# Optimization experiments

Hardware: AMD Instinct MI355X
Metric: run time of the kernel (lower is better)

The kernel has to match this reference:

```python
import jax, jax.numpy as jnp
from jax import lax
import numpy as np

B, T, D_IN, H, OUT = 64, 512, 512, 1024, 128


def setup_inputs() -> dict:
    key = jax.random.key(0)
    ks = jax.random.split(key, 12)
    s = 0.02
    return {
        "x": jax.random.normal(ks[0], (B, T, D_IN), dtype=jnp.float32),
        "W_ih0": jax.random.normal(ks[1], (H, D_IN), dtype=jnp.float32) * s,
        "W_hh0": jax.random.normal(ks[2], (H, H), dtype=jnp.float32) * s,
        "b_ih0": jax.random.normal(ks[3], (H,), dtype=jnp.float32) * s,
        "b_hh0": jax.random.normal(ks[4], (H,), dtype=jnp.float32) * s,
        "W_ih1": jax.random.normal(ks[5], (H, H), dtype=jnp.float32) * s,
        "W_hh1": jax.random.normal(ks[6], (H, H), dtype=jnp.float32) * s,
        "b_ih1": jax.random.normal(ks[7], (H,), dtype=jnp.float32) * s,
        "b_hh1": jax.random.normal(ks[8], (H,), dtype=jnp.float32) * s,
        "W_fc": jax.random.normal(ks[9], (OUT, H), dtype=jnp.float32) * s,
        "b_fc": jax.random.normal(ks[10], (OUT,), dtype=jnp.float32) * s,
    }


def _rnn_layer(seq, W_ih, W_hh, b_ih, b_hh):
    # seq: [B, T, D] -> outputs [B, T, H]; h_t = tanh(x_t W_ih^T + b_ih + h_{t-1} W_hh^T + b_hh)
    pre = jnp.einsum("btd,hd->bth", seq, W_ih) + b_ih + b_hh  # one big input GEMM
    h0 = jnp.zeros((seq.shape[0], W_hh.shape[0]), dtype=seq.dtype)

    def step(h, p_t):
        h_new = jnp.tanh(p_t + h @ W_hh.T)
        return h_new, h_new

    _, hs = lax.scan(step, h0, jnp.swapaxes(pre, 0, 1))  # [T, B, H]
    return jnp.swapaxes(hs, 0, 1)  # [B, T, H]


def reference(x, W_ih0, W_hh0, b_ih0, b_hh0, W_ih1, W_hh1, b_ih1, b_hh1, W_fc, b_fc):
    h1 = _rnn_layer(x, W_ih0, W_hh0, b_ih0, b_hh0)
    h2 = _rnn_layer(h1, W_ih1, W_hh1, b_ih1, b_hh1)
    last = h2[:, -1, :]  # [B, H]
    return last @ W_fc.T + b_fc  # [B, OUT]
```

## Files before the change

### kernel.cpp

```cpp
#include <hip/hip_runtime.h>
#include <stdint.h>
#include <stddef.h>

#define Bn   64
#define Tn   512
#define DINn 512
#define Hn   1024
#define OUTn 128

typedef __attribute__((ext_vector_type(4))) float f32x4;
typedef __attribute__((ext_vector_type(8))) short short8;
typedef __attribute__((ext_vector_type(4))) unsigned int u32x4;

__device__ __forceinline__ unsigned short f2bf(float f){
  unsigned int x = __builtin_bit_cast(unsigned int, f);
  x += 0x7fffu + ((x >> 16) & 1u);
  return (unsigned short)(x >> 16);
}
__device__ __forceinline__ float bf2f(unsigned short u){
  return __builtin_bit_cast(float, (unsigned int)u << 16);
}
__device__ __forceinline__ float tanh_fast(float v){
  float e = __expf(2.0f * v);
  return 1.0f - 2.0f / (e + 1.0f);
}

template<bool FAST>
__device__ __forceinline__ void st16(unsigned short* p, u32x4 v){
  if constexpr (FAST)
    asm volatile("global_store_dwordx4 %0, %1, off sc0" :: "v"(p), "v"(v) : "memory");
  else
    asm volatile("global_store_dwordx4 %0, %1, off sc0 sc1" :: "v"(p), "v"(v) : "memory");
}
__device__ __forceinline__ unsigned atom_poll(unsigned int* p){
  unsigned old, zero = 0;
  asm volatile("global_atomic_add %0, %1, %2, off sc0\n\t"
               "s_waitcnt vmcnt(0)"
               : "=&v"(old) : "v"(p), "v"(zero) : "memory");
  return old;
}
__device__ __forceinline__ void atom_poll2(unsigned int* p1, unsigned int* p2,
                                           unsigned &v1, unsigned &v2){
  unsigned zero = 0;
  asm volatile("global_atomic_add %0, %2, %4, off sc0\n\t"
               "global_atomic_add %1, %3, %4, off sc0\n\t"
               "s_waitcnt vmcnt(0)"
               : "=&v"(v1), "=&v"(v2)
               : "v"(p1), "v"(p2), "v"(zero) : "memory");
}
__device__ __forceinline__ void atom_inc(unsigned int* p){
  unsigned one = 1;
  asm volatile("global_atomic_add %0, %1, off" :: "v"(p), "v"(one) : "memory");
}
__device__ __forceinline__ unsigned ld1_sc0(const unsigned int* p){
  unsigned v;
  asm volatile("global_load_dword %0, %1, off sc0\n\t"
               "s_waitcnt vmcnt(0)" : "=&v"(v) : "v"(p) : "memory");
  return v;
}
__device__ __forceinline__ unsigned ld1_nt(const unsigned int* p){
  unsigned v;
  asm volatile("global_load_dword %0, %1, off nt\n\t"
               "s_waitcnt vmcnt(0)" : "=&v"(v) : "v"(p) : "memory");
  return v;
}
__device__ __forceinline__ unsigned umin4(u32x4 a){
  unsigned m0 = a[0] < a[1] ? a[0] : a[1];
  unsigned m1 = a[2] < a[3] ? a[2] : a[3];
  return m0 < m1 ? m0 : m1;
}
__device__ __forceinline__ unsigned ld_line8_nt(const unsigned int* p){
  u32x4 a, b;
  asm volatile("global_load_dwordx4 %0, %2, off nt\n\t"
               "global_load_dwordx4 %1, %3, off nt\n\t"
               "s_waitcnt vmcnt(0)"
               : "=&v"(a), "=&v"(b) : "v"(p), "v"(p + 4) : "memory");
  unsigned ma = umin4(a), mb = umin4(b);
  return ma < mb ? ma : mb;
}
__device__ __forceinline__ unsigned ld_line8_slow(const unsigned int* p){
  u32x4 a, b;
  asm volatile("global_load_dwordx4 %0, %2, off sc0 sc1\n\t"
               "global_load_dwordx4 %1, %3, off sc0 sc1\n\t"
               "s_waitcnt vmcnt(0)"
               : "=&v"(a), "=&v"(b) : "v"(p), "v"(p + 4) : "memory");
  unsigned ma = umin4(a), mb = umin4(b);
  return ma < mb ? ma : mb;
}
__device__ __forceinline__ void wait8_nt(const unsigned int* p, unsigned want){
  if (!want) return;
  for (int i = 0; i < (1 << 16); ++i){
    if (ld_line8_nt(p) >= want) return;
    if (i > 16) __builtin_amdgcn_s_sleep(1);
  }
}
__device__ __forceinline__ void wait8_nt2(const unsigned int* p1, unsigned w1,
                                          const unsigned int* p2, unsigned w2){
  if (!w1){ wait8_nt(p2, w2); return; }
  for (int i = 0; i < (1 << 16); ++i){
    u32x4 a, b, c, d;
    asm volatile("global_load_dwordx4 %0, %4, off nt\n\t"
                 "global_load_dwordx4 %1, %5, off nt\n\t"
                 "global_load_dwordx4 %2, %6, off nt\n\t"
                 "global_load_dwordx4 %3, %7, off nt\n\t"
                 "s_waitcnt vmcnt(0)"
                 : "=&v"(a), "=&v"(b), "=&v"(c), "=&v"(d)
                 : "v"(p1), "v"(p1 + 4), "v"(p2), "v"(p2 + 4) : "memory");
    unsigned m1 = umin4(a) < umin4(b) ? umin4(a) : umin4(b);
    unsigned m2 = umin4(c) < umin4(d) ? umin4(c) : umin4(d);
    if (m1 >= w1 && m2 >= w2) return;
    if (i > 16) __builtin_amdgcn_s_sleep(1);
  }
}
template<bool FAST>
__device__ __forceinline__ void wait_one(unsigned int* fc, unsigned int* fl, unsigned wfast, unsigned wslow){
  if constexpr (FAST){
    if (!wfast) return;
    for (int i = 0; i < (1 << 16); ++i){
      if (atom_poll(fc) >= wfast) return;
      if (i > 8) __builtin_amdgcn_s_sleep(1);
    }
  } else {
    if (!wslow) return;
    for (int i = 0; i < (1 << 16); ++i){
      if (ld_line8_slow(fl) >= wslow) return;
      if (i > 16) __builtin_amdgcn_s_sleep(1);
    }
  }
}
template<bool FAST>
__device__ __forceinline__ void wait_dual(unsigned int* fc1, unsigned int* fl1, unsigned wf1, unsigned ws1,
                                          unsigned int* fc2, unsigned int* fl2, unsigned wf2, unsigned ws2){
  if constexpr (FAST){
    if (!wf2){ wait_one<true>(fc1, fl1, wf1, ws1); return; }
    for (int i = 0; i < (1 << 16); ++i){
      unsigned v1, v2;
      atom_poll2(fc1, fc2, v1, v2);
      if (v1 >= wf1 && v2 >= wf2) return;
      if (i > 8) __builtin_amdgcn_s_sleep(1);
    }
  } else {
    if (!ws2){ wait_one<false>(fc1, fl1, wf1, ws1); return; }
    for (int i = 0; i < (1 << 16); ++i){
      if (ld_line8_slow(fl1) >= ws1 && ld_line8_slow(fl2) >= ws2) return;
      if (i > 16) __builtin_amdgcn_s_sleep(1);
    }
  }
}

__device__ __forceinline__ void stage_pw(const unsigned short* src, unsigned short* dst, int lane){
  const unsigned short* p0 = src + lane*8;
  const unsigned short* p1 = p0 + 512;
  u32x4 v0, v1;
  asm volatile("global_load_dwordx4 %0, %2, off sc0\n\t"
               "global_load_dwordx4 %1, %3, off sc0\n\t"
               "s_waitcnt vmcnt(0)"
               : "=&v"(v0), "=&v"(v1) : "v"(p0), "v"(p1) : "memory");
  *(u32x4*)(dst + lane*8) = v0;
  *(u32x4*)(dst + lane*8 + 512) = v1;
}
__device__ __forceinline__ void stage_pw_pv(const unsigned short* src, unsigned short* dst, int lane,
                                            const unsigned short* p4, float* pv){
  const unsigned short* p0 = src + lane*8;
  const unsigned short* p1 = p0 + 512;
  u32x4 v0, v1; unsigned u0,u1,u2,u3;
  asm volatile(
    "global_load_dwordx4 %0, %6, off sc0\n\t"
    "global_load_dwordx4 %1, %7, off sc0\n\t"
    "global_load_ushort %2, %8, off sc0\n\t"
    "global_load_ushort %3, %9, off sc0\n\t"
    "global_load_ushort %4, %10, off sc0\n\t"
    "global_load_ushort %5, %11, off sc0\n\t"
    "s_waitcnt vmcnt(0)"
    : "=&v"(v0),"=&v"(v1),"=&v"(u0),"=&v"(u1),"=&v"(u2),"=&v"(u3)
    : "v"(p0),"v"(p1),"v"(p4),"v"(p4+8),"v"(p4+16),"v"(p4+24) : "memory");
  *(u32x4*)(dst + lane*8) = v0;
  *(u32x4*)(dst + lane*8 + 512) = v1;
  pv[0]=bf2f((unsigned short)u0); pv[1]=bf2f((unsigned short)u1);
  pv[2]=bf2f((unsigned short)u2); pv[3]=bf2f((unsigned short)u3);
}

template<bool FAST>
__device__ __forceinline__ void stage_lin(const unsigned short* base, unsigned short* hl, int tid){
  const unsigned short* p0 = base + (size_t)tid * 8;
  const unsigned short* p1 = p0 + 4096;
  u32x4 v0, v1;
  if constexpr (FAST)
    asm volatile("global_load_dwordx4 %0, %2, off sc0\n\t"
                 "global_load_dwordx4 %1, %3, off sc0\n\t"
                 "s_waitcnt vmcnt(0)"
                 : "=&v"(v0), "=&v"(v1) : "v"(p0), "v"(p1) : "memory");
  else
    asm volatile("global_load_dwordx4 %0, %2, off sc0 sc1\n\t"
                 "global_load_dwordx4 %1, %3, off sc0 sc1\n\t"
                 "s_waitcnt vmcnt(0)"
                 : "=&v"(v0), "=&v"(v1) : "v"(p0), "v"(p1) : "memory");
  *(u32x4*)((char*)hl + tid * 16) = v0;
  *(u32x4*)((char*)hl + tid * 16 + 8192) = v1;
}
template<bool FAST>
__device__ __forceinline__ void ld4_chunk(const unsigned short* p, float* pv){
  unsigned u0,u1,u2,u3;
  if constexpr (FAST)
    asm volatile("global_load_ushort %0, %4, off sc0\n\t"
                 "global_load_ushort %1, %5, off sc0\n\t"
                 "global_load_ushort %2, %6, off sc0\n\t"
                 "global_load_ushort %3, %7, off sc0\n\t"
                 "s_waitcnt vmcnt(0)"
                 : "=&v"(u0), "=&v"(u1), "=&v"(u2), "=&v"(u3)
                 : "v"(p), "v"(p + 8), "v"(p + 16), "v"(p + 24) : "memory");
  else
    asm volatile("global_load_ushort %0, %4, off sc0 sc1\n\t"
                 "global_load_ushort %1, %5, off sc0 sc1\n\t"
                 "global_load_ushort %2, %6, off sc0 sc1\n\t"
                 "global_load_ushort %3, %7, off sc0 sc1\n\t"
                 "s_waitcnt vmcnt(0)"
                 : "=&v"(u0), "=&v"(u1), "=&v"(u2), "=&v"(u3)
                 : "v"(p), "v"(p + 8), "v"(p + 16), "v"(p + 24) : "memory");
  pv[0] = bf2f((unsigned short)u0); pv[1] = bf2f((unsigned short)u1);
  pv[2] = bf2f((unsigned short)u2); pv[3] = bf2f((unsigned short)u3);
}

__device__ __forceinline__ f32x4 mfma_tile(const char* lbase, const short8* wf, int lrow, int kh){
  f32x4 a0 = {0.f,0.f,0.f,0.f}, a1 = a0, a2 = a0, a3 = a0;
  int rb = kh * 128 + lrow * 16;
#pragma unroll
  for (int kk = 0; kk < 8; ++kk)
    a0 = __builtin_amdgcn_mfma_f32_16x16x32_bf16(*(const short8*)(lbase + kk*512 + rb), wf[kk], a0, 0,0,0);
#pragma unroll
  for (int kk = 8; kk < 16; ++kk)
    a1 = __builtin_amdgcn_mfma_f32_16x16x32_bf16(*(const short8*)(lbase + kk*512 + rb), wf[kk], a1, 0,0,0);
#pragma unroll
  for (int kk = 16; kk < 24; ++kk)
    a2 = __builtin_amdgcn_mfma_f32_16x16x32_bf16(*(const short8*)(lbase + kk*512 + rb), wf[kk], a2, 0,0,0);
#pragma unroll
  for (int kk = 24; kk < 32; ++kk)
    a3 = __builtin_amdgcn_mfma_f32_16x16x32_bf16(*(const short8*)(lbase + kk*512 + rb), wf[kk], a3, 0,0,0);
  return (a0 + a1) + (a2 + a3);
}

__global__ void cvt_bf16x8(const float* __restrict__ in, unsigned short* __restrict__ out,
                           long long n8){
  long long i = (long long)blockIdx.x * blockDim.x + threadIdx.x;
  long long stride = (long long)gridDim.x * blockDim.x;
  for (; i < n8; i += stride){
    const float* p = in + i*8;
    float4 a = *(const float4*)p;
    float4 b = *(const float4*)(p+4);
    short8 v;
    v[0]=(short)f2bf(a.x); v[1]=(short)f2bf(a.y); v[2]=(short)f2bf(a.z); v[3]=(short)f2bf(a.w);
    v[4]=(short)f2bf(b.x); v[5]=(short)f2bf(b.y); v[6]=(short)f2bf(b.z); v[7]=(short)f2bf(b.w);
    *(short8*)(out + i*8) = v;
  }
}

__global__ void bias_combine(const float* __restrict__ a, const float* __restrict__ b, float* __restrict__ o,
                             const float* __restrict__ c, const float* __restrict__ d, float* __restrict__ p){
  int i = blockIdx.x * blockDim.x + threadIdx.x;
  if (i < Hn){ o[i] = a[i] + b[i]; p[i] = c[i] + d[i]; }
}

__launch_bounds__(256, 2)
__global__ void gemm_pre0(const float* __restrict__ Av, const unsigned short* __restrict__ Bm,
                          const float* __restrict__ bias, unsigned short* __restrict__ C,
                          int N, int K)
{
  __shared__ unsigned short lA[128*64];
  __shared__ unsigned short lB[128*64];
  int bn = blockIdx.x, bm = blockIdx.y;
  int m0 = bm*128, n0 = bn*128;
  int tid = threadIdx.x, lane = tid & 63, w = tid >> 6;
  int wm = (w >> 1)*64, wn = (w & 1)*64;
  int cl = lane & 15, kh = lane >> 4;

  f32x4 acc[4][4];
  f32x4 z = {0.f,0.f,0.f,0.f};
#pragma unroll
  for (int i=0;i<4;i++)
#pragma unroll
    for (int j=0;j<4;j++) acc[i][j]=z;

  for (int k0 = 0; k0 < K; k0 += 64){
    __syncthreads();
#pragma unroll
    for (int r = 0; r < 4; ++r){
      int c = r*256 + tid;
      int row = c >> 3, cof = (c & 7)*8;
      const float* ap = Av + (size_t)(m0+row)*K + k0 + cof;
      float4 a = *(const float4*)ap;
      float4 b = *(const float4*)(ap+4);
      short8 v;
      v[0]=(short)f2bf(a.x); v[1]=(short)f2bf(a.y); v[2]=(short)f2bf(a.z); v[3]=(short)f2bf(a.w);
      v[4]=(short)f2bf(b.x); v[5]=(short)f2bf(b.y); v[6]=(short)f2bf(b.z); v[7]=(short)f2bf(b.w);
      *(short8*)&lA[row*64 + cof] = v;
      const unsigned short* bp = Bm + (size_t)(n0+row)*K + k0 + cof;
      *(short8*)&lB[row*64 + cof] = *(const short8*)bp;
    }
    __syncthreads();
#pragma unroll
    for (int kk = 0; kk < 2; ++kk){
      int kb = kk*32 + kh*8;
      short8 af[4], bfr[4];
#pragma unroll
      for (int i=0;i<4;i++) af[i]  = *(const short8*)&lA[(wm + i*16 + cl)*64 + kb];
#pragma unroll
      for (int j=0;j<4;j++) bfr[j] = *(const short8*)&lB[(wn + j*16 + cl)*64 + kb];
#pragma unroll
      for (int i=0;i<4;i++)
#pragma unroll
        for (int j=0;j<4;j++)
          acc[i][j] = __builtin_amdgcn_mfma_f32_16x16x32_bf16(af[i], bfr[j], acc[i][j], 0,0,0);
    }
  }
#pragma unroll
  for (int j=0;j<4;j++){
    int n = n0 + wn + j*16 + cl;
    float bs = bias[n];
#pragma unroll
    for (int i=0;i<4;i++){
      int mr = m0 + wm + i*16 + kh*4;
#pragma unroll
      for (int e=0;e<4;e++){
        int m = mr + e;
        int b = m >> 9, t = m & (Tn-1);
        C[((size_t)t*Bn + b)*N + n] = f2bf(acc[i][j][e] + bs);
      }
    }
  }
}

template<int MODE>
__device__ __forceinline__ void rnn_body(
    int role, int g, int slot, int tid, int w, int lane, int cl, int kh, int lrow,
    const unsigned short* pre0, unsigned short* bufP, unsigned short* h1buf,
    const float* bias1,
    unsigned int* FCA0, unsigned int* FCA1, unsigned int* FCB, unsigned int* FCC,
    unsigned int* FLA, unsigned int* FLB, unsigned int* FLC,
    unsigned int* FNA, unsigned int* FNB, unsigned int* FNC,
    const short8* wf, unsigned short* hl, unsigned short* outl)
{
  constexpr bool FAST = (MODE < 2);
  int n0 = slot*128 + w*16;
  int olocal = w*128 + ((cl>>3)*8 + kh*4)*8 + (cl&7);
  int khc = kh & 1;
  unsigned int* myFL = ((role == 0) ? FLA : (role == 1) ? FLB : FLC) + slot;
  unsigned int* myFN = ((role == 0) ? FNA : (role == 1) ? FNB : FNC) + slot*8 + w;

  for (int t = 0; t < Tn; ++t){
    unsigned short* hlb = (MODE == 0) ? hl + (t & 1)*8192 : hl;
    const char* lbase = (const char*)hlb;

    float pv[4] = {0.f,0.f,0.f,0.f};
    if (role == 0 && kh < 2){
      const unsigned short* pp = pre0 + ((size_t)t*Bn + g*8 + kh*4)*Hn + n0 + cl;
#pragma unroll
      for (int j=0;j<4;j++) pv[j] = bf2f(pp[(size_t)j*Hn]);
    }
    bool staged = true;
    if constexpr (MODE == 0){
      if (role == 0){
        if (t > 0){
          wait8_nt(FNA + w*8, (unsigned)t);
          stage_pw(h1buf + ((size_t)(t+1)*8 + g)*8192 + w*1024, hlb + w*1024, lane);
        } else staged = false;
      } else if (role == 1){
        wait8_nt(FNA + w*8, (unsigned)(t+1));
        stage_pw(h1buf + ((size_t)(t+2)*8 + g)*8192 + w*1024, hlb + w*1024, lane);
      } else {
        const unsigned short* pA = h1buf + ((size_t)t*8 + g)*8192 + slot*1024
                                   + ((w*16+cl)>>3)*64 + khc*32 + (cl&7);
        if (t > 0){
          wait8_nt2(FNC + w*8, (unsigned)t, FNB + slot*8, (unsigned)(t+1));
          stage_pw_pv(bufP + ((size_t)(t-1)*Bn + g*8)*Hn + w*1024, hlb + w*1024, lane, pA, pv);
        } else {
          staged = false;
          wait8_nt(FNB + slot*8, 1u);
          ld4_chunk<true>(pA, pv);
        }
      }
    } else {
      if (tid == 0){
        if (role == 0)      wait_one <FAST>(FCA0, FLA, 8u*(unsigned)t, (unsigned)t);
        else if (role == 1) wait_one <FAST>(FCA1, FLA, 8u*(unsigned)(t+1), (unsigned)(t+1));
        else                wait_dual<FAST>(FCB, FLB, 8u*(unsigned)(t+1), (unsigned)(t+1),
                                            FCC, FLC, 8u*(unsigned)t, (unsigned)t);
      }
      __syncthreads();
      if (role == 0){
        if (t > 0) stage_lin<FAST>(h1buf + ((size_t)(t+1)*8 + g)*8192, hlb, tid);
        else staged = false;
      } else if (role == 1){
        stage_lin<FAST>(h1buf + ((size_t)(t+2)*8 + g)*8192, hlb, tid);
      } else {
        if (kh < 2)
          ld4_chunk<FAST>(h1buf + ((size_t)t*8 + g)*8192 + slot*1024 + ((w*16+cl)>>3)*64 + kh*32 + (cl&7), pv);
        if (t > 0) stage_lin<FAST>(bufP + ((size_t)(t-1)*Bn + g*8)*Hn, hlb, tid);
        else staged = false;
      }
    }
    __syncthreads();
    f32x4 acc = {0.f,0.f,0.f,0.f};
    if (staged) acc = mfma_tile(lbase, wf, lrow, kh);
    if (kh < 2){
      float bs = (role == 1) ? bias1[n0 + cl] : 0.f;
#pragma unroll
      for (int j=0;j<4;j++){
        float v = acc[j] + pv[j] + bs;
        if (role != 1) v = tanh_fast(v);
        outl[olocal + j*8] = f2bf(v);
      }
    }
    unsigned short* tile;
    if (role == 0)      tile = h1buf + ((size_t)(t+2)*8 + g)*8192;
    else if (role == 1) tile = h1buf + ((size_t)t*8 + g)*8192;
    else                tile = bufP + ((size_t)t*Bn + g*8)*Hn;
    if (lane < 16){
      u32x4 v = *(const u32x4*)(outl + w*128 + lane*8);
      st16<FAST>(tile + slot*1024 + (w*16 + lane)*8, v);
    }
    if constexpr (MODE == 0){
      asm volatile("s_waitcnt vmcnt(0)" ::: "memory");
      if (lane == 0)
        asm volatile("global_store_dword %0, %1, off sc0" :: "v"(myFN), "v"((unsigned)(t+1)) : "memory");
    } else {
      asm volatile("s_waitcnt vmcnt(0)" ::: "memory");
      __syncthreads();
      if (tid == 0){
        if constexpr (MODE == 1){
          if (role == 0){ atom_inc(FCA0); atom_inc(FCA1); }
          else if (role == 1) atom_inc(FCB);
          else atom_inc(FCC);
        } else {
          asm volatile("global_store_dword %0, %1, off sc0 sc1" :: "v"(myFL), "v"((unsigned)(t+1)) : "memory");
        }
      }
    }
  }
}

__launch_bounds__(512, 2)
__global__ void rnn_fused(const unsigned short* __restrict__ pre0_ro,
                          unsigned short* __restrict__ bufP,
                          unsigned short* __restrict__ h1buf,
                          const float* __restrict__ Whh0,
                          const float* __restrict__ Wih1,
                          const float* __restrict__ Whh1,
                          const float* __restrict__ bias1,
                          unsigned int* ctrs)
{
  __shared__ __align__(16) unsigned short hl[16384];
  __shared__ __align__(16) unsigned short outl[1024];
  __shared__ int s_mode;
  int bx = blockIdx.x;
  int g = bx & 7;
  int sub = bx >> 3;
  int role = sub >> 3, slot = sub & 7;
  int tid = threadIdx.x, lane = tid & 63, w = tid >> 6;
  int n0 = slot*128 + w*16;
  int cl = lane & 15, kh = lane >> 4, lrow = cl & 7;
  unsigned int* FLA = ctrs + (0*8 + g)*32;
  unsigned int* FLB = ctrs + (1*8 + g)*32;
  unsigned int* FLC = ctrs + (2*8 + g)*32;
  unsigned int* arrive1 = ctrs + 768;
  unsigned int* badAT   = ctrs + 772;
  unsigned int* arrive2 = ctrs + 776;
  unsigned int* badNT   = ctrs + 780;
  unsigned int* arrive3 = ctrs + 784;
  unsigned int* FCA0 = ctrs + 1536 + (0*8 + g)*32;
  unsigned int* FCB  = ctrs + 1536 + (1*8 + g)*32;
  unsigned int* FCC  = ctrs + 1536 + (2*8 + g)*32;
  unsigned int* FCA1 = ctrs + 1536 + (3*8 + g)*32;
  unsigned int* FNA = ctrs + 2560 + (0*8 + g)*64;
  unsigned int* FNB = ctrs + 2560 + (1*8 + g)*64;
  unsigned int* FNC = ctrs + 2560 + (2*8 + g)*64;

  if (tid == 0){
    int xcc;
    asm volatile("s_getreg_b32 %0, hwreg(HW_REG_XCC_ID)" : "=s"(xcc));
    unsigned int* atw = ctrs + 1024 + g*32;  unsigned int* atarmed = atw + 16;
    unsigned int* ntw = ctrs + 1280 + g*32;  unsigned int* ntarmed = ntw + 16;
    if (xcc != g){
      __hip_atomic_fetch_or(badNT, 1u, __ATOMIC_RELAXED, __HIP_MEMORY_SCOPE_AGENT);
      __hip_atomic_fetch_or(badAT, 1u, __ATOMIC_RELAXED, __HIP_MEMORY_SCOPE_AGENT);
    }
    unsigned pr = ld1_nt(ntw) + ld1_nt(ntarmed);
    asm volatile("" :: "v"(pr));
    __hip_atomic_fetch_add(arrive1, 1u, __ATOMIC_ACQ_REL, __HIP_MEMORY_SCOPE_AGENT);
    int t1 = 0;
    for (int i = 0; i < (1 << 20); ++i){
      if (__hip_atomic_load(arrive1, __ATOMIC_ACQUIRE, __HIP_MEMORY_SCOPE_AGENT) >= 192u){ t1 = 1; break; }
      __builtin_amdgcn_s_sleep(2);
    }
    if (!t1){
      __hip_atomic_fetch_or(badNT, 1u, __ATOMIC_RELAXED, __HIP_MEMORY_SCOPE_AGENT);
      __hip_atomic_fetch_or(badAT, 1u, __ATOMIC_RELAXED, __HIP_MEMORY_SCOPE_AGENT);
    }
    unsigned magicN = 0xBEEF0000u | (unsigned)g;
    if (sub == 0){
      asm volatile("global_store_dword %0, %1, off sc0\n\t"
                   "s_waitcnt vmcnt(0)\n\t"
                   "global_store_dword %2, %3, off sc0"
                   :: "v"(ntw), "v"(magicN), "v"(ntarmed), "v"(1u) : "memory");
    }
    int okN = 0;
    for (int i = 0; i < (1 << 14); ++i){
      if (ld1_nt(ntarmed) == 1u){ okN = (ld1_nt(ntw) == magicN); break; }
      if (i > 8) __builtin_amdgcn_s_sleep(1);
    }
    if (!okN) __hip_atomic_fetch_or(badNT, 1u, __ATOMIC_RELAXED, __HIP_MEMORY_SCOPE_AGENT);
    __hip_atomic_fetch_add(arrive2, 1u, __ATOMIC_ACQ_REL, __HIP_MEMORY_SCOPE_AGENT);
    int t2 = 0;
    for (int i = 0; i < (1 << 20); ++i){
      if (__hip_atomic_load(arrive2, __ATOMIC_ACQUIRE, __HIP_MEMORY_SCOPE_AGENT) >= 192u){ t2 = 1; break; }
      __builtin_amdgcn_s_sleep(2);
    }
    if (!t2){
      __hip_atomic_fetch_or(badNT, 1u, __ATOMIC_RELAXED, __HIP_MEMORY_SCOPE_AGENT);
      __hip_atomic_fetch_or(badAT, 1u, __ATOMIC_RELAXED, __HIP_MEMORY_SCOPE_AGENT);
    }
    unsigned magicA = 0xCAFE0000u | (unsigned)g;
    if (sub == 0){
      asm volatile("global_store_dword %0, %1, off sc0\n\t"
                   "s_waitcnt vmcnt(0)" :: "v"(atw), "v"(magicA) : "memory");
      atom_inc(atarmed);
    }
    int okA = 0;
    for (int i = 0; i < (1 << 15); ++i){
      if (atom_poll(atarmed) >= 1u){ okA = (ld1_sc0(atw) == magicA); break; }
      if (i > 16) __builtin_amdgcn_s_sleep(1);
    }
    if (!okA) __hip_atomic_fetch_or(badAT, 1u, __ATOMIC_RELAXED, __HIP_MEMORY_SCOPE_AGENT);
    __hip_atomic_fetch_add(arrive3, 1u, __ATOMIC_ACQ_REL, __HIP_MEMORY_SCOPE_AGENT);
    int t3 = 0;
    for (int i = 0; i < (1 << 20); ++i){
      if (__hip_atomic_load(arrive3, __ATOMIC_ACQUIRE, __HIP_MEMORY_SCOPE_AGENT) >= 192u){ t3 = 1; break; }
      __builtin_amdgcn_s_sleep(2);
    }
    unsigned bN = __hip_atomic_load(badNT, __ATOMIC_ACQUIRE, __HIP_MEMORY_SCOPE_AGENT);
    unsigned bA = __hip_atomic_load(badAT, __ATOMIC_ACQUIRE, __HIP_MEMORY_SCOPE_AGENT);
    s_mode = (!t3) ? 2 : (bN == 0u ? 0 : (bA == 0u ? 1 : 2));
  }
  __syncthreads();
  const int mode = s_mode;

  const float* Wmat = (role == 0) ? Whh0 : (role == 1) ? Wih1 : Whh1;
  short8 wf[32];
  {
    const float* wr = Wmat + (size_t)(n0 + cl)*Hn + kh*8;
#pragma unroll
    for (int kk = 0; kk < 32; ++kk){
      float4 a = *(const float4*)(wr + kk*32);
      float4 b = *(const float4*)(wr + kk*32 + 4);
      short8 v;
      v[0]=(short)f2bf(a.x); v[1]=(short)f2bf(a.y); v[2]=(short)f2bf(a.z); v[3]=(short)f2bf(a.w);
      v[4]=(short)f2bf(b.x); v[5]=(short)f2bf(b.y); v[6]=(short)f2bf(b.z); v[7]=(short)f2bf(b.w);
      wf[kk] = v;
    }
  }

  if (mode == 0)
    rnn_body<0>(role, g, slot, tid, w, lane, cl, kh, lrow, pre0_ro, bufP, h1buf,
                bias1, FCA0, FCA1, FCB, FCC, FLA, FLB, FLC, FNA, FNB, FNC, wf, hl, outl);
  else if (mode == 1)
    rnn_body<1>(role, g, slot, tid, w, lane, cl, kh, lrow, pre0_ro, bufP, h1buf,
                bias1, FCA0, FCA1, FCB, FCC, FLA, FLB, FLC, FNA, FNB, FNC, wf, hl, outl);
  else
    rnn_body<2>(role, g, slot, tid, w, lane, cl, kh, lrow, pre0_ro, bufP, h1buf,
                bias1, FCA0, FCA1, FCB, FCC, FLA, FLB, FLC, FNA, FNB, FNC, wf, hl, outl);
}

__global__ void fc_k(const unsigned short* __restrict__ bufP,
                     const float* __restrict__ Wfc, const float* __restrict__ bfc,
                     float* __restrict__ out)
{
  int gw = (blockIdx.x * blockDim.x + threadIdx.x) >> 6;
  int lane = threadIdx.x & 63;
  int b = gw >> 7, o = gw & 127;
  const unsigned short* tile = bufP + ((size_t)(Tn-1)*Bn + (b & ~7))*Hn;
  int r = b & 7;
  const float* wr = Wfc + (size_t)o*Hn;
  float s = 0.f;
  for (int k = lane; k < Hn; k += 64)
    s += bf2f(tile[((k>>3)*8 + r)*8 + (k&7)]) * wr[k];
#pragma unroll
  for (int off = 32; off > 0; off >>= 1) s += __shfl_down(s, off, 64);
  if (lane == 0) out[b*OUTn + o] = s + bfc[o];
}

extern "C" void kernel_launch(void* const* d_in, const int* in_sizes, int n_in,
                              void* d_out, int out_size, void* d_ws, size_t ws_size,
                              hipStream_t stream)
{
  const float* x    = (const float*)d_in[0];
  const float* Wih0 = (const float*)d_in[1];
  const float* Whh0 = (const float*)d_in[2];
  const float* bih0 = (const float*)d_in[3];
  const float* bhh0 = (const float*)d_in[4];
  const float* Wih1 = (const float*)d_in[5];
  const float* Whh1 = (const float*)d_in[6];
  const float* bih1 = (const float*)d_in[7];
  const float* bhh1 = (const float*)d_in[8];
  const float* Wfc  = (const float*)d_in[9];
  const float* bfc  = (const float*)d_in[10];
  float* out = (float*)d_out;

  unsigned short* bufP  = (unsigned short*)d_ws;
  unsigned short* h1buf = bufP  + (size_t)Bn*Tn*Hn;
  unsigned short* wih0b = h1buf + (size_t)(Tn+2)*8*8192;
  float* bias0 = (float*)(wih0b + (size_t)Hn*DINn);
  float* bias1 = bias0 + Hn;
  unsigned int* ctrs = (unsigned int*)(bias1 + Hn);

  hipMemsetAsync(ctrs, 0, 4096*sizeof(unsigned int), stream);

  cvt_bf16x8<<<256, 256, 0, stream>>>(Wih0, wih0b, (long long)Hn*DINn/8);
  bias_combine<<<4, 256, 0, stream>>>(bih0, bhh0, bias0, bih1, bhh1, bias1);

  dim3 g1(Hn/128, (Bn*Tn)/128);
  gemm_pre0<<<g1, 256, 0, stream>>>(x, wih0b, bias0, bufP, Hn, DINn);

  rnn_fused<<<192, 512, 0, stream>>>(bufP, bufP, h1buf, Whh0, Wih1, Whh1, bias1, ctrs);

  fc_k<<<2048, 256, 0, stream>>>(bufP, Wfc, bfc, out);
}
```

Measured before the change: 1.127 ms.

## Halve waves per RNN block, each wave computing two 16-column tiles

The persistent RNN kernel now launches 256 threads per block instead of 512. Each of the 4 waves holds two sets of bf16 weight fragments and computes 32 output columns through interleaved MFMA chains. Staging loads widen to four dwordx4 per lane, and the per-wave flag layout and polling shrink to match. This cuts the number of waves that sync and poll per step, but doubles register pressure for the weights (64 short8 per lane) and lengthens each wave's serial MFMA work.

```diff
diff --git a/kernel.cpp b/kernel.cpp
--- a/kernel.cpp
+++ b/kernel.cpp
@@ -87,6 +87,13 @@
   unsigned ma = umin4(a), mb = umin4(b);
   return ma < mb ? ma : mb;
 }
+__device__ __forceinline__ void waitw_nt(const unsigned int* p, unsigned want){
+  if (!want) return;
+  for (int i = 0; i < (1 << 16); ++i){
+    if (ld1_nt(p) >= want) return;
+    if (i > 16) __builtin_amdgcn_s_sleep(1);
+  }
+}
 __device__ __forceinline__ void wait8_nt(const unsigned int* p, unsigned want){
   if (!want) return;
   for (int i = 0; i < (1 << 16); ++i){
@@ -94,21 +101,18 @@
     if (i > 16) __builtin_amdgcn_s_sleep(1);
   }
 }
-__device__ __forceinline__ void wait8_nt2(const unsigned int* p1, unsigned w1,
-                                          const unsigned int* p2, unsigned w2){
-  if (!w1){ wait8_nt(p2, w2); return; }
+__device__ __forceinline__ void waitC_nt(const unsigned int* pline, unsigned wline,
+                                         const unsigned int* pw, unsigned ww){
   for (int i = 0; i < (1 << 16); ++i){
-    u32x4 a, b, c, d;
-    asm volatile("global_load_dwordx4 %0, %4, off nt\n\t"
-                 "global_load_dwordx4 %1, %5, off nt\n\t"
-                 "global_load_dwordx4 %2, %6, off nt\n\t"
-                 "global_load_dwordx4 %3, %7, off nt\n\t"
+    u32x4 a, b; unsigned v;
+    asm volatile("global_load_dwordx4 %0, %3, off nt\n\t"
+                 "global_load_dwordx4 %1, %4, off nt\n\t"
+                 "global_load_dword %2, %5, off nt\n\t"
                  "s_waitcnt vmcnt(0)"
-                 : "=&v"(a), "=&v"(b), "=&v"(c), "=&v"(d)
-                 : "v"(p1), "v"(p1 + 4), "v"(p2), "v"(p2 + 4) : "memory");
-    unsigned m1 = umin4(a) < umin4(b) ? umin4(a) : umin4(b);
-    unsigned m2 = umin4(c) < umin4(d) ? umin4(c) : umin4(d);
-    if (m1 >= w1 && m2 >= w2) return;
+                 : "=&v"(a), "=&v"(b), "=&v"(v)
+                 : "v"(pline), "v"(pline + 4), "v"(pw) : "memory");
+    unsigned m = umin4(a) < umin4(b) ? umin4(a) : umin4(b);
+    if (m >= wline && v >= ww) return;
     if (i > 16) __builtin_amdgcn_s_sleep(1);
   }
 }
@@ -148,55 +152,79 @@
   }
 }
 
-__device__ __forceinline__ void stage_pw(const unsigned short* src, unsigned short* dst, int lane){
+__device__ __forceinline__ void stage_pw4k(const unsigned short* src, unsigned short* dst, int lane){
   const unsigned short* p0 = src + lane*8;
-  const unsigned short* p1 = p0 + 512;
-  u32x4 v0, v1;
-  asm volatile("global_load_dwordx4 %0, %2, off sc0\n\t"
-               "global_load_dwordx4 %1, %3, off sc0\n\t"
+  u32x4 v0, v1, v2, v3;
+  asm volatile("global_load_dwordx4 %0, %4, off sc0\n\t"
+               "global_load_dwordx4 %1, %5, off sc0\n\t"
+               "global_load_dwordx4 %2, %6, off sc0\n\t"
+               "global_load_dwordx4 %3, %7, off sc0\n\t"
                "s_waitcnt vmcnt(0)"
-               : "=&v"(v0), "=&v"(v1) : "v"(p0), "v"(p1) : "memory");
+               : "=&v"(v0), "=&v"(v1), "=&v"(v2), "=&v"(v3)
+               : "v"(p0), "v"(p0 + 512), "v"(p0 + 1024), "v"(p0 + 1536) : "memory");
   *(u32x4*)(dst + lane*8) = v0;
   *(u32x4*)(dst + lane*8 + 512) = v1;
-}
-__device__ __forceinline__ void stage_pw_pv(const unsigned short* src, unsigned short* dst, int lane,
-                                            const unsigned short* p4, float* pv){
+  *(u32x4*)(dst + lane*8 + 1024) = v2;
+  *(u32x4*)(dst + lane*8 + 1536) = v3;
+}
+__device__ __forceinline__ void stage_pw4k_pv(const unsigned short* src, unsigned short* dst, int lane,
+                                              const unsigned short* pA, const unsigned short* pB,
+                                              float* pvA, float* pvB){
   const unsigned short* p0 = src + lane*8;
-  const unsigned short* p1 = p0 + 512;
-  u32x4 v0, v1; unsigned u0,u1,u2,u3;
+  u32x4 v0, v1, v2, v3;
+  unsigned a0,a1,a2,a3,b0,b1,b2,b3;
   asm volatile(
-    "global_load_dwordx4 %0, %6, off sc0\n\t"
-    "global_load_dwordx4 %1, %7, off sc0\n\t"
-    "global_load_ushort %2, %8, off sc0\n\t"
-    "global_load_ushort %3, %9, off sc0\n\t"
-    "global_load_ushort %4, %10, off sc0\n\t"
-    "global_load_ushort %5, %11, off sc0\n\t"
+    "global_load_dwordx4 %0, %12, off sc0\n\t"
+    "global_load_dwordx4 %1, %13, off sc0\n\t"
+    "global_load_dwordx4 %2, %14, off sc0\n\t"
+    "global_load_dwordx4 %3, %15, off sc0\n\t"
+    "global_load_ushort %4, %16, off sc0\n\t"
+    "global_load_ushort %5, %17, off sc0\n\t"
+    "global_load_ushort %6, %18, off sc0\n\t"
+    "global_load_ushort %7, %19, off sc0\n\t"
+    "global_load_ushort %8, %20, off sc0\n\t"
+    "global_load_ushort %9, %21, off sc0\n\t"
+    "global_load_ushort %10, %22, off sc0\n\t"
+    "global_load_ushort %11, %23, off sc0\n\t"
     "s_waitcnt vmcnt(0)"
-    : "=&v"(v0),"=&v"(v1),"=&v"(u0),"=&v"(u1),"=&v"(u2),"=&v"(u3)
-    : "v"(p0),"v"(p1),"v"(p4),"v"(p4+8),"v"(p4+16),"v"(p4+24) : "memory");
+    : "=&v"(v0),"=&v"(v1),"=&v"(v2),"=&v"(v3),
+      "=&v"(a0),"=&v"(a1),"=&v"(a2),"=&v"(a3),"=&v"(b0),"=&v"(b1),"=&v"(b2),"=&v"(b3)
+    : "v"(p0), "v"(p0+512), "v"(p0+1024), "v"(p0+1536),
+      "v"(pA),"v"(pA+8),"v"(pA+16),"v"(pA+24),
+      "v"(pB),"v"(pB+8),"v"(pB+16),"v"(pB+24) : "memory");
   *(u32x4*)(dst + lane*8) = v0;
   *(u32x4*)(dst + lane*8 + 512) = v1;
-  pv[0]=bf2f((unsigned short)u0); pv[1]=bf2f((unsigned short)u1);
-  pv[2]=bf2f((unsigned short)u2); pv[3]=bf2f((unsigned short)u3);
-}
-
+  *(u32x4*)(dst + lane*8 + 1024) = v2;
+  *(u32x4*)(dst + lane*8 + 1536) = v3;
+  pvA[0]=bf2f((unsigned short)a0); pvA[1]=bf2f((unsigned short)a1);
+  pvA[2]=bf2f((unsigned short)a2); pvA[3]=bf2f((unsigned short)a3);
+  pvB[0]=bf2f((unsigned short)b0); pvB[1]=bf2f((unsigned short)b1);
+  pvB[2]=bf2f((unsigned short)b2); pvB[3]=bf2f((unsigned short)b3);
+}
 template<bool FAST>
-__device__ __forceinline__ void stage_lin(const unsigned short* base, unsigned short* hl, int tid){
+__device__ __forceinline__ void stage_lin4(const unsigned short* base, unsigned short* hl, int tid){
   const unsigned short* p0 = base + (size_t)tid * 8;
-  const unsigned short* p1 = p0 + 4096;
-  u32x4 v0, v1;
+  u32x4 v0, v1, v2, v3;
   if constexpr (FAST)
-    asm volatile("global_load_dwordx4 %0, %2, off sc0\n\t"
-                 "global_load_dwordx4 %1, %3, off sc0\n\t"
+    asm volatile("global_load_dwordx4 %0, %4, off sc0\n\t"
+                 "global_load_dwordx4 %1, %5, off sc0\n\t"
+                 "global_load_dwordx4 %2, %6, off sc0\n\t"
+                 "global_load_dwordx4 %3, %7, off sc0\n\t"
                  "s_waitcnt vmcnt(0)"
-                 : "=&v"(v0), "=&v"(v1) : "v"(p0), "v"(p1) : "memory");
+                 : "=&v"(v0), "=&v"(v1), "=&v"(v2), "=&v"(v3)
+                 : "v"(p0), "v"(p0+2048), "v"(p0+4096), "v"(p0+6144) : "memory");
   else
-    asm volatile("global_load_dwordx4 %0, %2, off sc0 sc1\n\t"
-                 "global_load_dwordx4 %1, %3, off sc0 sc1\n\t"
+    asm volatile("global_load_dwordx4 %0, %4, off sc0 sc1\n\t"
+                 "global_load_dwordx4 %1, %5, off sc0 sc1\n\t"
+                 "global_load_dwordx4 %2, %6, off sc0 sc1\n\t"
+                 "global_load_dwordx4 %3, %7, off sc0 sc1\n\t"
                  "s_waitcnt vmcnt(0)"
-                 : "=&v"(v0), "=&v"(v1) : "v"(p0), "v"(p1) : "memory");
-  *(u32x4*)((char*)hl + tid * 16) = v0;
-  *(u32x4*)((char*)hl + tid * 16 + 8192) = v1;
+                 : "=&v"(v0), "=&v"(v1), "=&v"(v2), "=&v"(v3)
+                 : "v"(p0), "v"(p0+2048), "v"(p0+4096), "v"(p0+6144) : "memory");
+  *(u32x4*)(hl + tid*8) = v0;
+  *(u32x4*)(hl + tid*8 + 2048) = v1;
+  *(u32x4*)(hl + tid*8 + 4096) = v2;
+  *(u32x4*)(hl + tid*8 + 6144) = v3;
 }
 template<bool FAST>
 __device__ __forceinline__ void ld4_chunk(const unsigned short* p, float* pv){
@@ -221,22 +249,21 @@
   pv[2] = bf2f((unsigned short)u2); pv[3] = bf2f((unsigned short)u3);
 }
 
-__device__ __forceinline__ f32x4 mfma_tile(const char* lbase, const short8* wf, int lrow, int kh){
-  f32x4 a0 = {0.f,0.f,0.f,0.f}, a1 = a0, a2 = a0, a3 = a0;
+__device__ __forceinline__ void mfma_tile2(const char* lbase, const short8* wfA, const short8* wfB,
+                                           int lrow, int kh, f32x4& outA, f32x4& outB){
+  f32x4 z = {0.f,0.f,0.f,0.f};
+  f32x4 a0 = z, a1 = z, b0 = z, b1 = z;
   int rb = kh * 128 + lrow * 16;
 #pragma unroll
-  for (int kk = 0; kk < 8; ++kk)
-    a0 = __builtin_amdgcn_mfma_f32_16x16x32_bf16(*(const short8*)(lbase + kk*512 + rb), wf[kk], a0, 0,0,0);
-#pragma unroll
-  for (int kk = 8; kk < 16; ++kk)
-    a1 = __builtin_amdgcn_mfma_f32_16x16x32_bf16(*(const short8*)(lbase + kk*512 + rb), wf[kk], a1, 0,0,0);
-#pragma unroll
-  for (int kk = 16; kk < 24; ++kk)
-    a2 = __builtin_amdgcn_mfma_f32_16x16x32_bf16(*(const short8*)(lbase + kk*512 + rb), wf[kk], a2, 0,0,0);
-#pragma unroll
-  for (int kk = 24; kk < 32; ++kk)
-    a3 = __builtin_amdgcn_mfma_f32_16x16x32_bf16(*(const short8*)(lbase + kk*512 + rb), wf[kk], a3, 0,0,0);
-  return (a0 + a1) + (a2 + a3);
+  for (int kk = 0; kk < 32; kk += 2){
+    short8 x = *(const short8*)(lbase + kk*512 + rb);
+    short8 y = *(const short8*)(lbase + (kk+1)*512 + rb);
+    a0 = __builtin_amdgcn_mfma_f32_16x16x32_bf16(x, wfA[kk],   a0, 0,0,0);
+    b0 = __builtin_amdgcn_mfma_f32_16x16x32_bf16(x, wfB[kk],   b0, 0,0,0);
+    a1 = __builtin_amdgcn_mfma_f32_16x16x32_bf16(y, wfA[kk+1], a1, 0,0,0);
+    b1 = __builtin_amdgcn_mfma_f32_16x16x32_bf16(y, wfB[kk+1], b1, 0,0,0);
+  }
+  outA = a0 + a1; outB = b0 + b1;
 }
 
 __global__ void cvt_bf16x8(const float* __restrict__ in, unsigned short* __restrict__ out,
@@ -337,45 +364,50 @@
     unsigned int* FCA0, unsigned int* FCA1, unsigned int* FCB, unsigned int* FCC,
     unsigned int* FLA, unsigned int* FLB, unsigned int* FLC,
     unsigned int* FNA, unsigned int* FNB, unsigned int* FNC,
-    const short8* wf, unsigned short* hl, unsigned short* outl)
+    const short8* wfA, const short8* wfB, unsigned short* hl, unsigned short* outl)
 {
   constexpr bool FAST = (MODE < 2);
-  int n0 = slot*128 + w*16;
-  int olocal = w*128 + ((cl>>3)*8 + kh*4)*8 + (cl&7);
+  int c0 = slot*128 + 32*w;
+  int olocal = w*256 + ((cl>>3)*8 + kh*4)*8 + (cl&7);
   int khc = kh & 1;
   unsigned int* myFL = ((role == 0) ? FLA : (role == 1) ? FLB : FLC) + slot;
-  unsigned int* myFN = ((role == 0) ? FNA : (role == 1) ? FNB : FNC) + slot*8 + w;
+  unsigned int* myFN = ((role == 0) ? FNA : (role == 1) ? FNB : FNC) + slot*4 + w;
+
+  float bsA = 0.f, bsB = 0.f;
+  if (role == 1){ bsA = bias1[c0 + cl]; bsB = bias1[c0 + 16 + cl]; }
 
   for (int t = 0; t < Tn; ++t){
     unsigned short* hlb = (MODE == 0) ? hl + (t & 1)*8192 : hl;
     const char* lbase = (const char*)hlb;
 
-    float pv[4] = {0.f,0.f,0.f,0.f};
+    float pvA[4] = {0.f,0.f,0.f,0.f}, pvB[4] = {0.f,0.f,0.f,0.f};
     if (role == 0 && kh < 2){
-      const unsigned short* pp = pre0 + ((size_t)t*Bn + g*8 + kh*4)*Hn + n0 + cl;
-#pragma unroll
-      for (int j=0;j<4;j++) pv[j] = bf2f(pp[(size_t)j*Hn]);
+      const unsigned short* pp = pre0 + ((size_t)t*Bn + g*8 + kh*4)*Hn + c0 + cl;
+#pragma unroll
+      for (int j=0;j<4;j++){ pvA[j] = bf2f(pp[(size_t)j*Hn]); pvB[j] = bf2f(pp[(size_t)j*Hn + 16]); }
     }
     bool staged = true;
     if constexpr (MODE == 0){
       if (role == 0){
         if (t > 0){
           wait8_nt(FNA + w*8, (unsigned)t);
-          stage_pw(h1buf + ((size_t)(t+1)*8 + g)*8192 + w*1024, hlb + w*1024, lane);
+          stage_pw4k(h1buf + ((size_t)(t+1)*8 + g)*8192 + 2*w*1024, hlb + 2*w*1024, lane);
         } else staged = false;
       } else if (role == 1){
         wait8_nt(FNA + w*8, (unsigned)(t+1));
-        stage_pw(h1buf + ((size_t)(t+2)*8 + g)*8192 + w*1024, hlb + w*1024, lane);
+        stage_pw4k(h1buf + ((size_t)(t+2)*8 + g)*8192 + 2*w*1024, hlb + 2*w*1024, lane);
       } else {
-        const unsigned short* pA = h1buf + ((size_t)t*8 + g)*8192 + slot*1024
-                                   + ((w*16+cl)>>3)*64 + khc*32 + (cl&7);
+        const unsigned short* pb = h1buf + ((size_t)t*8 + g)*8192 + slot*1024;
+        const unsigned short* pA = pb + ((c0 - slot*128 + cl) >> 3)*64 + khc*32 + (cl & 7);
+        const unsigned short* pB = pA + 128;
         if (t > 0){
-          wait8_nt2(FNC + w*8, (unsigned)t, FNB + slot*8, (unsigned)(t+1));
-          stage_pw_pv(bufP + ((size_t)(t-1)*Bn + g*8)*Hn + w*1024, hlb + w*1024, lane, pA, pv);
+          waitC_nt(FNC + w*8, (unsigned)t, FNB + slot*4 + w, (unsigned)(t+1));
+          stage_pw4k_pv(bufP + ((size_t)(t-1)*Bn + g*8)*Hn + 2*w*1024, hlb + 2*w*1024, lane,
+                        pA, pB, pvA, pvB);
         } else {
           staged = false;
-          wait8_nt(FNB + slot*8, 1u);
-          ld4_chunk<true>(pA, pv);
+          waitw_nt(FNB + slot*4 + w, 1u);
+          ld4_chunk<true>(pA, pvA); ld4_chunk<true>(pB, pvB);
         }
       }
     } else {
@@ -387,36 +419,39 @@
       }
       __syncthreads();
       if (role == 0){
-        if (t > 0) stage_lin<FAST>(h1buf + ((size_t)(t+1)*8 + g)*8192, hlb, tid);
+        if (t > 0) stage_lin4<FAST>(h1buf + ((size_t)(t+1)*8 + g)*8192, hlb, tid);
         else staged = false;
       } else if (role == 1){
-        stage_lin<FAST>(h1buf + ((size_t)(t+2)*8 + g)*8192, hlb, tid);
+        stage_lin4<FAST>(h1buf + ((size_t)(t+2)*8 + g)*8192, hlb, tid);
       } else {
-        if (kh < 2)
-          ld4_chunk<FAST>(h1buf + ((size_t)t*8 + g)*8192 + slot*1024 + ((w*16+cl)>>3)*64 + kh*32 + (cl&7), pv);
-        if (t > 0) stage_lin<FAST>(bufP + ((size_t)(t-1)*Bn + g*8)*Hn, hlb, tid);
+        const unsigned short* pb = h1buf + ((size_t)t*8 + g)*8192 + slot*1024;
+        const unsigned short* pA = pb + ((32*w + cl) >> 3)*64 + kh*32 + (cl & 7);
+        if (kh < 2){ ld4_chunk<FAST>(pA, pvA); ld4_chunk<FAST>(pA + 128, pvB); }
+        if (t > 0) stage_lin4<FAST>(bufP + ((size_t)(t-1)*Bn + g*8)*Hn, hlb, tid);
         else staged = false;
       }
     }
     __syncthreads();
-    f32x4 acc = {0.f,0.f,0.f,0.f};
-    if (staged) acc = mfma_tile(lbase, wf, lrow, kh);
+    f32x4 accA = {0.f,0.f,0.f,0.f}, accB = accA;
+    if (staged) mfma_tile2(lbase, wfA, wfB, lrow, kh, accA, accB);
     if (kh < 2){
-      float bs = (role == 1) ? bias1[n0 + cl] : 0.f;
 #pragma unroll
       for (int j=0;j<4;j++){
-        float v = acc[j] + pv[j] + bs;
-        if (role != 1) v = tanh_fast(v);
-        outl[olocal + j*8] = f2bf(v);
+        float vA = accA[j] + pvA[j] + bsA;
+        float vB = accB[j] + pvB[j] + bsB;
+        if (role != 1){ vA = tanh_fast(vA); vB = tanh_fast(vB); }
+        outl[olocal + j*8]       = f2bf(vA);
+        outl[olocal + 128 + j*8] = f2bf(vB);
       }
     }
     unsigned short* tile;
     if (role == 0)      tile = h1buf + ((size_t)(t+2)*8 + g)*8192;
     else if (role == 1) tile = h1buf + ((size_t)t*8 + g)*8192;
     else                tile = bufP + ((size_t)t*Bn + g*8)*Hn;
+    tile += slot*1024;
     if (lane < 16){
-      u32x4 v = *(const u32x4*)(outl + w*128 + lane*8);
-      st16<FAST>(tile + slot*1024 + (w*16 + lane)*8, v);
+      st16<FAST>(tile + (32*w + lane)*8,      *(const u32x4*)(outl + w*256 + lane*8));
+      st16<FAST>(tile + (32*w + 16 + lane)*8, *(const u32x4*)(outl + w*256 + 128 + lane*8));
     }
     if constexpr (MODE == 0){
       asm volatile("s_waitcnt vmcnt(0)" ::: "memory");
@@ -438,7 +473,7 @@
   }
 }
 
-__launch_bounds__(512, 2)
+__launch_bounds__(256, 1)
 __global__ void rnn_fused(const unsigned short* __restrict__ pre0_ro,
                           unsigned short* __restrict__ bufP,
                           unsigned short* __restrict__ h1buf,
@@ -456,7 +491,6 @@
   int sub = bx >> 3;
   int role = sub >> 3, slot = sub & 7;
   int tid = threadIdx.x, lane = tid & 63, w = tid >> 6;
-  int n0 = slot*128 + w*16;
   int cl = lane & 15, kh = lane >> 4, lrow = cl & 7;
   unsigned int* FLA = ctrs + (0*8 + g)*32;
   unsigned int* FLB = ctrs + (1*8 + g)*32;
@@ -470,9 +504,9 @@
   unsigned int* FCB  = ctrs + 1536 + (1*8 + g)*32;
   unsigned int* FCC  = ctrs + 1536 + (2*8 + g)*32;
   unsigned int* FCA1 = ctrs + 1536 + (3*8 + g)*32;
-  unsigned int* FNA = ctrs + 2560 + (0*8 + g)*64;
-  unsigned int* FNB = ctrs + 2560 + (1*8 + g)*64;
-  unsigned int* FNC = ctrs + 2560 + (2*8 + g)*64;
+  unsigned int* FNA = ctrs + 2560 + (0*8 + g)*32;
+  unsigned int* FNB = ctrs + 2560 + (1*8 + g)*32;
+  unsigned int* FNC = ctrs + 2560 + (2*8 + g)*32;
 
   if (tid == 0){
     int xcc;
@@ -544,29 +578,41 @@
   const int mode = s_mode;
 
   const float* Wmat = (role == 0) ? Whh0 : (role == 1) ? Wih1 : Whh1;
-  short8 wf[32];
+  int c0 = slot*128 + 32*w;
+  short8 wfA[32], wfB[32];
   {
-    const float* wr = Wmat + (size_t)(n0 + cl)*Hn + kh*8;
+    const float* wrA = Wmat + (size_t)(c0 + cl)*Hn + kh*8;
+    const float* wrB = wrA + (size_t)16*Hn;
 #pragma unroll
     for (int kk = 0; kk < 32; ++kk){
-      float4 a = *(const float4*)(wr + kk*32);
-      float4 b = *(const float4*)(wr + kk*32 + 4);
-      short8 v;
-      v[0]=(short)f2bf(a.x); v[1]=(short)f2bf(a.y); v[2]=(short)f2bf(a.z); v[3]=(short)f2bf(a.w);
-      v[4]=(short)f2bf(b.x); v[5]=(short)f2bf(b.y); v[6]=(short)f2bf(b.z); v[7]=(short)f2bf(b.w);
-      wf[kk] = v;
+      {
+        float4 a = *(const float4*)(wrA + kk*32);
+        float4 b = *(const float4*)(wrA + kk*32 + 4);
+        short8 v;
+        v[0]=(short)f2bf(a.x); v[1]=(short)f2bf(a.y); v[2]=(short)f2bf(a.z); v[3]=(short)f2bf(a.w);
+        v[4]=(short)f2bf(b.x); v[5]=(short)f2bf(b.y); v[6]=(short)f2bf(b.z); v[7]=(short)f2bf(b.w);
+        wfA[kk] = v;
+      }
+      {
+        float4 a = *(const float4*)(wrB + kk*32);
+        float4 b = *(const float4*)(wrB + kk*32 + 4);
+        short8 v;
+        v[0]=(short)f2bf(a.x); v[1]=(short)f2bf(a.y); v[2]=(short)f2bf(a.z); v[3]=(short)f2bf(a.w);
+        v[4]=(short)f2bf(b.x); v[5]=(short)f2bf(b.y); v[6]=(short)f2bf(b.z); v[7]=(short)f2bf(b.w);
+        wfB[kk] = v;
+      }
     }
   }
 
   if (mode == 0)
     rnn_body<0>(role, g, slot, tid, w, lane, cl, kh, lrow, pre0_ro, bufP, h1buf,
-                bias1, FCA0, FCA1, FCB, FCC, FLA, FLB, FLC, FNA, FNB, FNC, wf, hl, outl);
+                bias1, FCA0, FCA1, FCB, FCC, FLA, FLB, FLC, FNA, FNB, FNC, wfA, wfB, hl, outl);
   else if (mode == 1)
     rnn_body<1>(role, g, slot, tid, w, lane, cl, kh, lrow, pre0_ro, bufP, h1buf,
-                bias1, FCA0, FCA1, FCB, FCC, FLA, FLB, FLC, FNA, FNB, FNC, wf, hl, outl);
+                bias1, FCA0, FCA1, FCB, FCC, FLA, FLB, FLC, FNA, FNB, FNC, wfA, wfB, hl, outl);
   else
     rnn_body<2>(role, g, slot, tid, w, lane, cl, kh, lrow, pre0_ro, bufP, h1buf,
-                bias1, FCA0, FCA1, FCB, FCC, FLA, FLB, FLC, FNA, FNB, FNC, wf, hl, outl);
+                bias1, FCA0, FCA1, FCB, FCC, FLA, FLB, FLC, FNA, FNB, FNC, wfA, wfB, hl, outl);
 }
 
 __global__ void fc_k(const unsigned short* __restrict__ bufP,
@@ -619,7 +665,7 @@
   dim3 g1(Hn/128, (Bn*Tn)/128);
   gemm_pre0<<<g1, 256, 0, stream>>>(x, wih0b, bias0, bufP, Hn, DINn);
 
-  rnn_fused<<<192, 512, 0, stream>>>(bufP, bufP, h1buf, Whh0, Wih1, Whh1, bias1, ctrs);
+  rnn_fused<<<192, 256, 0, stream>>>(bufP, bufP, h1buf, Whh0, Wih1, Whh1, bias1, ctrs);
 
   fc_k<<<2048, 256, 0, stream>>>(bufP, Wfc, bfc, out);
 }
```

After: 1.423 ms. 1.26x slower.
